# Kernel optimization log

Measured on AMD Instinct MI355X. Metric: run time of the kernel, lower is better.

The kernel has to match this reference:

```python
import jax, jax.numpy as jnp
import numpy as np

EPS = float(np.finfo(np.float32).eps)

# (joint_id, joint_name, parent_name) in the module's fkm_computation_order
ORDER = [
    (1, 'rHip', 'hip'), (2, 'rKnee', 'rHip'), (3, 'rAnkle', 'rKnee'), (4, 'rToe', 'rAnkle'),
    (6, 'lHip', 'hip'), (7, 'lKnee', 'lHip'), (8, 'lAnkle', 'lKnee'), (9, 'lToe', 'lAnkle'),
    (11, 'spine', 'hip'), (12, 'spine1', 'spine'), (13, 'thorax', 'spine1'), (14, 'neck', 'thorax'),
    (15, 'head', 'neck'), (16, 'lShoulderAnchor', 'spine1'), (17, 'lShoulder', 'lShoulderAnchor'),
    (18, 'lElbow', 'lShoulder'), (19, 'lWrist', 'lElbow'), (20, 'lThumb', 'lWrist'),
    (22, 'lWristEnd', 'lWrist'), (24, 'rShoulderAnchor', 'spine1'), (25, 'rShoulder', 'rShoulderAnchor'),
    (26, 'rElbow', 'rShoulder'), (27, 'rWrist', 'rElbow'), (28, 'rThumb', 'rWrist'),
    (30, 'rWristEnd', 'rWrist'),
]


def axis_angle_to_matrix(a):
    """Rodrigues formula, batched. a: [B,3] -> [B,3,3]."""
    theta = jnp.linalg.norm(a, axis=-1, keepdims=True)  # [B,1]
    r = a / (theta + EPS)                               # [B,3]
    r0, r1, r2 = r[:, 0], r[:, 1], r[:, 2]
    z = jnp.zeros_like(r0)
    # skew-symmetric S with S[0,1]=-r2, S[0,2]=r1, S[1,2]=-r0 (as in torch code)
    S = jnp.stack([
        jnp.stack([z, -r2, r1], axis=-1),
        jnp.stack([r2, z, -r0], axis=-1),
        jnp.stack([-r1, r0, z], axis=-1),
    ], axis=-2)  # [B,3,3]
    th = theta[..., None]  # [B,1,1]
    I = jnp.eye(3, dtype=a.dtype)
    return I + jnp.sin(th) * S + (1.0 - jnp.cos(th)) * (S @ S)


def setup_inputs() -> dict:
    key = jax.random.key(0)
    k1, k2 = jax.random.split(key)
    B = 262144
    x = jax.random.normal(k1, (B, 99), dtype=jnp.float32)
    offset = jax.random.normal(k2, (32, 3), dtype=jnp.float32)
    return {"x": x, "offset": offset}


def reference(x, offset):
    # hip root: position from first 3 dims, orientation from dims 3:6
    pos = {"hip": offset[0] + x[:, 0:3]}                # [B,3]
    ang = {"hip": axis_angle_to_matrix(x[:, 3:6])}      # [B,3,3]
    # local rotations for every joint in the chain: dims [3*id+3 : 3*id+6]
    local = {name: axis_angle_to_matrix(x[:, 3 * i + 3: 3 * i + 6]) for i, name, _ in ORDER}
    # sequential forward kinematics down the tree
    for i, cur, par in ORDER:
        # offset[i] @ R_parent  (row-vector times matrix), then translate
        pos[cur] = jnp.einsum('j,bjk->bk', offset[i], ang[par]) + pos[par]
        ang[cur] = local[cur] @ ang[par]
    # positions in the same order as get_joint_positions(): hip then chain order
    return jnp.stack([pos['hip']] + [pos[c] for _, c, _ in ORDER], axis=1)  # [B,26,3]
```

## Files before the change

### kernel.cpp

```cpp
#include <hip/hip_runtime.h>

#define TPB  256
#define RPW  64
#define XDIM 99
#define NJ   26
#define OUTW 78

constexpr int OFF_IDX[NJ] = {0,1,2,3,4,6,7,8,9,11,12,13,14,15,16,17,18,19,20,22,24,25,26,27,28,30};
constexpr int PAR[NJ]     = {-1,0,1,2,3,0,5,6,7,0,9,10,11,12,10,14,15,16,17,17,10,20,21,22,23,23};

__device__ __forceinline__ float fast_rcp(float a)  { return __builtin_amdgcn_rcpf(a); }
__device__ __forceinline__ float fast_sqrt(float a) { return __builtin_amdgcn_sqrtf(a); }

__device__ __forceinline__ void rodrigues(float ax, float ay, float az, float* R) {
    const float EPS = 1.1920928955078125e-07f;
    float xx = ax*ax, yy = ay*ay, zz = az*az;
    float t = fast_sqrt(xx + yy + zz);
    float inv = fast_rcp(t + EPS);
    float s, c;
    __sincosf(t, &s, &c);
    float k1 = s * inv;
    float k2 = (1.0f - c) * (inv * inv);
    float xy = ax*ay, xz = ax*az, yz = ay*az;
    R[0] = 1.0f - k2*(yy + zz);
    R[1] = -k1*az + k2*xy;
    R[2] =  k1*ay + k2*xz;
    R[3] =  k1*az + k2*xy;
    R[4] = 1.0f - k2*(xx + zz);
    R[5] = -k1*ax + k2*yz;
    R[6] = -k1*ay + k2*xz;
    R[7] =  k1*ax + k2*yz;
    R[8] = 1.0f - k2*(xx + yy);
}

#define STEP(s) do {                                                          \
    const int i_  = OFF_IDX[(s)];                                             \
    const int pa_ = PAR[(s)];                                                 \
    float L[9];                                                               \
    rodrigues(row[3*i_+3], row[3*i_+4], row[3*i_+5], L);                      \
    const float o0 = off[3*i_], o1 = off[3*i_+1], o2 = off[3*i_+2];           \
    _Pragma("unroll")                                                         \
    for (int c = 0; c < 3; ++c)                                               \
        pp[(s)][c] = o0*ang[pa_][c] + o1*ang[pa_][3+c] + o2*ang[pa_][6+c]     \
                   + pp[pa_][c];                                              \
    _Pragma("unroll")                                                         \
    for (int j = 0; j < 3; ++j)                                               \
        _Pragma("unroll")                                                     \
        for (int kk = 0; kk < 3; ++kk)                                        \
            ang[(s)][3*j+kk] = L[3*j+0]*ang[pa_][0+kk]                        \
                             + L[3*j+1]*ang[pa_][3+kk]                        \
                             + L[3*j+2]*ang[pa_][6+kk];                       \
} while (0)

__global__ __launch_bounds__(TPB, 4) void skel_fk(const float* __restrict__ x,
                                                  const float* __restrict__ off,
                                                  float* __restrict__ out) {
    __shared__ __align__(16) float buf[RPW * XDIM];
    const int t = threadIdx.x;
    const int w = t >> 6;
    const int l = t & 63;
    const int row0 = blockIdx.x * RPW;
    const float* gsrc = x + (long long)row0 * XDIM;

    #pragma unroll
    for (int j = 0; j < 6; ++j) {
        const int jj = 6 * w + j;
        __builtin_amdgcn_global_load_lds(
            (const __attribute__((address_space(1))) unsigned int*)(gsrc + 256*jj + 4*l),
            (__attribute__((address_space(3))) unsigned int*)(buf + 256*jj),
            16, 0, 0);
    }
    if (w >= 1) {
        const int kk = w - 1;
        __builtin_amdgcn_global_load_lds(
            (const __attribute__((address_space(1))) unsigned int*)(gsrc + 6144 + 64*kk + l),
            (__attribute__((address_space(3))) unsigned int*)(buf + 6144 + 64*kk),
            4, 0, 0);
    }
    __syncthreads();

    const float* row = &buf[l * XDIM];
    float ang[NJ][9];
    float pp[NJ][3];

    {
        float R[9];
        rodrigues(row[3], row[4], row[5], R);
        #pragma unroll
        for (int q = 0; q < 9; ++q) ang[0][q] = R[q];
        pp[0][0] = off[0] + row[0];
        pp[0][1] = off[1] + row[1];
        pp[0][2] = off[2] + row[2];
    }

    if (w == 0) {
        #pragma unroll
        for (int s = 1; s <= 8; ++s) STEP(s);
    } else if (w == 1) {
        #pragma unroll
        for (int s = 9; s <= 13; ++s) STEP(s);
    } else if (w == 2) {
        STEP(9); STEP(10);
        #pragma unroll
        for (int s = 14; s <= 19; ++s) STEP(s);
    } else {
        STEP(9); STEP(10);
        #pragma unroll
        for (int s = 20; s <= 25; ++s) STEP(s);
    }
    __syncthreads();

    {
        float* srow = &buf[l * OUTW];
        if (w == 0) {
            #pragma unroll
            for (int s = 1; s <= 8; ++s) {
                srow[3*s+0] = pp[s][0]; srow[3*s+1] = pp[s][1]; srow[3*s+2] = pp[s][2];
            }
        } else if (w == 1) {
            srow[0] = pp[0][0]; srow[1] = pp[0][1]; srow[2] = pp[0][2];
            #pragma unroll
            for (int s = 9; s <= 13; ++s) {
                srow[3*s+0] = pp[s][0]; srow[3*s+1] = pp[s][1]; srow[3*s+2] = pp[s][2];
            }
        } else if (w == 2) {
            #pragma unroll
            for (int s = 14; s <= 19; ++s) {
                srow[3*s+0] = pp[s][0]; srow[3*s+1] = pp[s][1]; srow[3*s+2] = pp[s][2];
            }
        } else {
            #pragma unroll
            for (int s = 20; s <= 25; ++s) {
                srow[3*s+0] = pp[s][0]; srow[3*s+1] = pp[s][1]; srow[3*s+2] = pp[s][2];
            }
        }
    }
    __syncthreads();

    {
        float4* ob4 = reinterpret_cast<float4*>(out + (long long)row0 * OUTW);
        const float4* b4 = reinterpret_cast<const float4*>(buf);
        #pragma unroll
        for (int j = 0; j < 4; ++j)
            ob4[t + 256*j] = b4[t + 256*j];
        if (t < 224) ob4[1024 + t] = b4[1024 + t];
    }
}

extern "C" void kernel_launch(void* const* d_in, const int* in_sizes, int n_in,
                              void* d_out, int out_size, void* d_ws, size_t ws_size,
                              hipStream_t stream) {
    const float* x   = (const float*)d_in[0];
    const float* off = (const float*)d_in[1];
    float* out = (float*)d_out;
    const int B = in_sizes[0] / XDIM;
    const int grid = B / RPW;
    skel_fk<<<grid, TPB, 0, stream>>>(x, off, out);
}
```

Measured before the change: 35.99 us.

## Warp-specialize kernel with triple-buffered LDS slabs to overlap DMA, compute and stores

Each block now handles 8 slabs of 64 rows using 512 threads. Four waves compute forward kinematics while the other four waves prefetch the next slab into LDS with global_load_lds and flush the previous slab's outputs, rotating through three LDS buffers. The aim is to hide global memory latency behind compute, where before each block loaded, computed and stored in sequence. In exchange the grid is 8x smaller, LDS per block roughly triples, which limits how many blocks fit per CU, and half of the waves never do arithmetic.

```diff
diff --git a/kernel.cpp b/kernel.cpp
--- a/kernel.cpp
+++ b/kernel.cpp
@@ -1,10 +1,12 @@
 #include <hip/hip_runtime.h>
 
-#define TPB  256
-#define RPW  64
+#define TPB  512
+#define RPS  64
+#define NSL  8
 #define XDIM 99
 #define NJ   26
 #define OUTW 78
+#define SLABF (RPS * XDIM)
 
 constexpr int OFF_IDX[NJ] = {0,1,2,3,4,6,7,8,9,11,12,13,14,15,16,17,18,19,20,22,24,25,26,27,28,30};
 constexpr int PAR[NJ]     = {-1,0,1,2,3,0,5,6,7,0,9,10,11,12,10,14,15,16,17,17,10,20,21,22,23,23};
@@ -52,99 +54,126 @@
                              + L[3*j+2]*ang[pa_][6+kk];                       \
 } while (0)
 
+__device__ __forceinline__ void dma_slab(const float* gsrc, float* lbuf, int wio, int l) {
+    #pragma unroll
+    for (int j = 0; j < 6; ++j) {
+        const int jj = 6 * wio + j;
+        __builtin_amdgcn_global_load_lds(
+            (const __attribute__((address_space(1))) unsigned int*)(gsrc + 256*jj + 4*l),
+            (__attribute__((address_space(3))) unsigned int*)(lbuf + 256*jj),
+            16, 0, 0);
+    }
+    if (wio >= 1) {
+        const int kk = wio - 1;
+        __builtin_amdgcn_global_load_lds(
+            (const __attribute__((address_space(1))) unsigned int*)(gsrc + 6144 + 64*kk + l),
+            (__attribute__((address_space(3))) unsigned int*)(lbuf + 6144 + 64*kk),
+            4, 0, 0);
+    }
+}
+
+__device__ __forceinline__ void flush_slab(const float* slab, float* ob, int g) {
+    const float4* b4 = reinterpret_cast<const float4*>(slab);
+    float4* ob4 = reinterpret_cast<float4*>(ob);
+    float4 v0 = b4[g], v1 = b4[g+256], v2 = b4[g+512], v3 = b4[g+768];
+    ob4[g]     = v0; ob4[g+256] = v1;
+    ob4[g+512] = v2; ob4[g+768] = v3;
+    if (g < 224) {
+        float4 v4 = b4[g + 1024];
+        ob4[g + 1024] = v4;
+    }
+}
+
 __global__ __launch_bounds__(TPB, 4) void skel_fk(const float* __restrict__ x,
                                                   const float* __restrict__ off,
                                                   float* __restrict__ out) {
-    __shared__ __align__(16) float buf[RPW * XDIM];
+    __shared__ __align__(16) float bufs[3][SLABF];
     const int t = threadIdx.x;
     const int w = t >> 6;
     const int l = t & 63;
-    const int row0 = blockIdx.x * RPW;
-    const float* gsrc = x + (long long)row0 * XDIM;
+    const int wio = (w >= 4) ? (w - 4) : 0;
+    const int g = (wio << 6) | l;
+    const long long row0 = (long long)blockIdx.x * (NSL * RPS);
+    const float* gx = x + row0 * XDIM;
+    float* ox = out + row0 * OUTW;
 
-    #pragma unroll
-    for (int j = 0; j < 6; ++j) {
-        const int jj = 6 * w + j;
-        __builtin_amdgcn_global_load_lds(
-            (const __attribute__((address_space(1))) unsigned int*)(gsrc + 256*jj + 4*l),
-            (__attribute__((address_space(3))) unsigned int*)(buf + 256*jj),
-            16, 0, 0);
-    }
-    if (w >= 1) {
-        const int kk = w - 1;
-        __builtin_amdgcn_global_load_lds(
-            (const __attribute__((address_space(1))) unsigned int*)(gsrc + 6144 + 64*kk + l),
-            (__attribute__((address_space(3))) unsigned int*)(buf + 6144 + 64*kk),
-            4, 0, 0);
-    }
+    if (w >= 4) dma_slab(gx, bufs[0], wio, l);
     __syncthreads();
 
-    const float* row = &buf[l * XDIM];
-    float ang[NJ][9];
-    float pp[NJ][3];
+    int ci = 0, ni = 1, oi = 2;
 
-    {
-        float R[9];
-        rodrigues(row[3], row[4], row[5], R);
-        #pragma unroll
-        for (int q = 0; q < 9; ++q) ang[0][q] = R[q];
-        pp[0][0] = off[0] + row[0];
-        pp[0][1] = off[1] + row[1];
-        pp[0][2] = off[2] + row[2];
+    #pragma unroll 1
+    for (int k = 0; k < NSL; ++k) {
+        float* cur = bufs[ci];
+        float pp[NJ][3];
+
+        if (w < 4) {
+            const float* row = &cur[l * XDIM];
+            float ang[NJ][9];
+            {
+                float R[9];
+                rodrigues(row[3], row[4], row[5], R);
+                #pragma unroll
+                for (int q = 0; q < 9; ++q) ang[0][q] = R[q];
+                pp[0][0] = off[0] + row[0];
+                pp[0][1] = off[1] + row[1];
+                pp[0][2] = off[2] + row[2];
+            }
+            if (w == 0) {
+                #pragma unroll
+                for (int s = 1; s <= 8; ++s) STEP(s);
+            } else if (w == 1) {
+                #pragma unroll
+                for (int s = 9; s <= 13; ++s) STEP(s);
+            } else if (w == 2) {
+                STEP(9); STEP(10);
+                #pragma unroll
+                for (int s = 14; s <= 19; ++s) STEP(s);
+            } else {
+                STEP(9); STEP(10);
+                #pragma unroll
+                for (int s = 20; s <= 25; ++s) STEP(s);
+            }
+        } else {
+            if (k + 1 < NSL)
+                dma_slab(gx + (long long)(k + 1) * SLABF, bufs[ni], wio, l);
+            if (k > 0)
+                flush_slab(bufs[oi], ox + (long long)(k - 1) * RPS * OUTW, g);
+        }
+        __syncthreads();
+
+        if (w < 4) {
+            float* srow = &cur[l * OUTW];
+            if (w == 0) {
+                #pragma unroll
+                for (int s = 1; s <= 8; ++s) {
+                    srow[3*s+0]=pp[s][0]; srow[3*s+1]=pp[s][1]; srow[3*s+2]=pp[s][2];
+                }
+            } else if (w == 1) {
+                srow[0]=pp[0][0]; srow[1]=pp[0][1]; srow[2]=pp[0][2];
+                #pragma unroll
+                for (int s = 9; s <= 13; ++s) {
+                    srow[3*s+0]=pp[s][0]; srow[3*s+1]=pp[s][1]; srow[3*s+2]=pp[s][2];
+                }
+            } else if (w == 2) {
+                #pragma unroll
+                for (int s = 14; s <= 19; ++s) {
+                    srow[3*s+0]=pp[s][0]; srow[3*s+1]=pp[s][1]; srow[3*s+2]=pp[s][2];
+                }
+            } else {
+                #pragma unroll
+                for (int s = 20; s <= 25; ++s) {
+                    srow[3*s+0]=pp[s][0]; srow[3*s+1]=pp[s][1]; srow[3*s+2]=pp[s][2];
+                }
+            }
+        }
+        __syncthreads();
+
+        const int tmp = oi; oi = ci; ci = ni; ni = tmp;
     }
 
-    if (w == 0) {
-        #pragma unroll
-        for (int s = 1; s <= 8; ++s) STEP(s);
-    } else if (w == 1) {
-        #pragma unroll
-        for (int s = 9; s <= 13; ++s) STEP(s);
-    } else if (w == 2) {
-        STEP(9); STEP(10);
-        #pragma unroll
-        for (int s = 14; s <= 19; ++s) STEP(s);
-    } else {
-        STEP(9); STEP(10);
-        #pragma unroll
-        for (int s = 20; s <= 25; ++s) STEP(s);
-    }
-    __syncthreads();
-
-    {
-        float* srow = &buf[l * OUTW];
-        if (w == 0) {
-            #pragma unroll
-            for (int s = 1; s <= 8; ++s) {
-                srow[3*s+0] = pp[s][0]; srow[3*s+1] = pp[s][1]; srow[3*s+2] = pp[s][2];
-            }
-        } else if (w == 1) {
-            srow[0] = pp[0][0]; srow[1] = pp[0][1]; srow[2] = pp[0][2];
-            #pragma unroll
-            for (int s = 9; s <= 13; ++s) {
-                srow[3*s+0] = pp[s][0]; srow[3*s+1] = pp[s][1]; srow[3*s+2] = pp[s][2];
-            }
-        } else if (w == 2) {
-            #pragma unroll
-            for (int s = 14; s <= 19; ++s) {
-                srow[3*s+0] = pp[s][0]; srow[3*s+1] = pp[s][1]; srow[3*s+2] = pp[s][2];
-            }
-        } else {
-            #pragma unroll
-            for (int s = 20; s <= 25; ++s) {
-                srow[3*s+0] = pp[s][0]; srow[3*s+1] = pp[s][1]; srow[3*s+2] = pp[s][2];
-            }
-        }
-    }
-    __syncthreads();
-
-    {
-        float4* ob4 = reinterpret_cast<float4*>(out + (long long)row0 * OUTW);
-        const float4* b4 = reinterpret_cast<const float4*>(buf);
-        #pragma unroll
-        for (int j = 0; j < 4; ++j)
-            ob4[t + 256*j] = b4[t + 256*j];
-        if (t < 224) ob4[1024 + t] = b4[1024 + t];
-    }
+    if (w >= 4)
+        flush_slab(bufs[oi], ox + (long long)(NSL - 1) * RPS * OUTW, g);
 }
 
 extern "C" void kernel_launch(void* const* d_in, const int* in_sizes, int n_in,
@@ -154,6 +183,6 @@
     const float* off = (const float*)d_in[1];
     float* out = (float*)d_out;
     const int B = in_sizes[0] / XDIM;
-    const int grid = B / RPW;
+    const int grid = B / (NSL * RPS);
     skel_fk<<<grid, TPB, 0, stream>>>(x, off, out);
 }
```

Result: slower. 131.3 us (+265.0%).
